# Kernel tuning notes

Hardware: AMD Instinct MI355X
Metric: run time of the kernel (lower is better)

## Reference

```python
import jax, jax.numpy as jnp
import numpy as np

NEARZERO = 1e-6
UH_LEN = 15
T_STEPS, N_GRID, NMUL = 1460, 2000, 1

BOUNDS = [
    ("inf_pc", 0.0, 1.0), ("inf_hbv_beta", 0.5, 3.0), ("inf_vic_bexp", 0.001, 3.0),
    ("inf_hmets_alpha", 0.3, 1.0), ("bf1_gr4j_x3", 20.0, 300.0), ("bf1_bfc", -8.0, -2.0),
    ("bf1_bfn", 1.0, 5.0), ("bf1_bfmax", 0.1, 200.0), ("bf1_lam", 0.1, 0.5),
    ("bf1_thresh", 0.0001, 0.9999), ("max_perc", 1.0, 50.0), ("perc_sfc", 0.0001, 0.9999),
    ("crise_hbv", 0.1, 50.0), ("bf2_bfmax", 0.1, 100.0), ("bf2_gr4j_x3", 50.0, 500.0),
    ("bf2_bfc", -8.0, -2.0), ("bf2_bfn", 1.0, 5.0), ("Tbf", -5.0, 2.0), ("Kf", 0.0, 5.0),
    ("ddf_min", 1.5, 3.0), ("ddf_plus", 0.0, 5.0), ("Kcum", 0.01, 0.2), ("Tbm", -1.0, 1.0),
    ("swi", 0.0, 0.4), ("forest_cover", 0.0, 1.0), ("forest_sparseness", 0.0, 1.0),
    ("max_soilwater1", 50.0, 500.0), ("max_soilwater2", 50.0, 500.0),
    ("alpha1", 0.3, 20.0), ("beta1", 0.01, 5.0), ("alpha2", 0.5, 13.0), ("beta2", 0.15, 1.5),
]


def setup_inputs():
    key = jax.random.key(0)
    kP, kT, kE, kW, kH = jax.random.split(key, 5)
    prcp = jnp.maximum(jax.random.normal(kP, (T_STEPS, N_GRID)) * 8.0, 0.0)  # mm/day
    temp = jax.random.normal(kT, (T_STEPS, N_GRID)) * 10.0                   # degC
    pet = jax.random.uniform(kE, (T_STEPS, N_GRID)) * 5.0                    # mm/day
    x_phy = jnp.stack([prcp, temp, pet], axis=-1).astype(jnp.float32)
    weights_params = jax.random.normal(kW, (T_STEPS, N_GRID, 24), dtype=jnp.float32)
    hybrid_params = jax.random.normal(kH, (N_GRID, 32), dtype=jnp.float32)
    return {"x_phy": x_phy, "weights_params": weights_params, "hybrid_params": hybrid_params}


def _route(flow, alpha, beta):
    # flow [T,G,M]; alpha,beta [G,M]. Discrete gamma-shaped causal unit hydrograph.
    k = jnp.arange(1.0, UH_LEN + 1.0, dtype=flow.dtype)
    logw = (alpha[..., None] - 1.0) * jnp.log(k) - k / beta[..., None]  # [G,M,L]
    uh = jax.nn.softmax(logw, axis=-1)
    out = jnp.zeros_like(flow)
    for lag in range(UH_LEN):  # small fixed UH length
        shifted = jnp.pad(flow, ((lag, 0), (0, 0), (0, 0)))[: flow.shape[0]]
        out = out + uh[..., lag] * shifted
    return out


def _forward(x_phy, weights_params, hybrid_params):
    T, G, _ = x_phy.shape
    # --- unpack + descale parameters (sigmoid -> physical range) ---
    s = jax.nn.sigmoid(hybrid_params.reshape(G, len(BOUNDS), NMUL))
    p = {n: lo + s[:, i] * (hi - lo) for i, (n, lo, hi) in enumerate(BOUNDS)}  # each [G,M]
    w = weights_params.reshape(T, G, 24, NMUL)
    w_inf = jax.nn.softmax(w[:, :, 0:6], axis=2)    # infiltration blend weights
    w_bf1 = jax.nn.softmax(w[:, :, 6:12], axis=2)   # baseflow1 blend weights
    w_bf2 = jax.nn.softmax(w[:, :, 12:18], axis=2)  # baseflow2 blend weights
    gates = jnp.round(jax.nn.sigmoid(w[:, :, 18:24]))  # perc,capi,evpr,evps,conv1,conv2
    Pm, Tm, Petm = x_phy[:, :, 0:1], x_phy[:, :, 1:2], x_phy[:, :, 2:3]

    def step(carry, xs):
        snow, liq, cum, sw1, sw2 = carry
        prcp, temp, pet, wi, wb1, wb2, g = xs
        rain = jnp.where(temp >= 0.0, prcp, 0.0)
        snowf = jnp.where(temp < 0.0, prcp, 0.0)
        canopy = pet * p["forest_cover"] * (1.0 - p["forest_sparseness"])
        rain = jnp.maximum(rain - canopy * g[:, 2], 0.0)
        snowf = jnp.maximum(snowf - canopy * g[:, 3], 0.0)
        # HBV refreeze of snowpack liquid water
        refreeze = jnp.minimum(liq, p["Kf"] * jnp.maximum(p["Tbf"] - temp, 0.0))
        snow = snow + snowf + refreeze
        liq = liq - refreeze
        # HMETS degree-day melt with cumulative-melt-dependent factor
        ddf = p["ddf_min"] + p["ddf_plus"] * (1.0 - jnp.exp(-p["Kcum"] * cum))
        melt = jnp.minimum(snow, ddf * jnp.maximum(temp - p["Tbm"], 0.0))
        snow = snow - melt
        cum = jnp.where(snow < NEARZERO, NEARZERO, cum + melt)
        liq = liq + melt
        overflow = jnp.maximum(liq - p["swi"] * snow, 0.0)  # snow liquid retention
        liq = liq - overflow
        wavail = rain + overflow
        # blended infiltration (6 options)
        sat1 = jnp.clip(sw1 / p["max_soilwater1"], NEARZERO, 1.0)
        dry1 = jnp.clip(1.0 - sat1, NEARZERO, 1.0)
        inf_opts = jnp.stack([
            wavail * p["inf_pc"],
            wavail * (1.0 - sat1 ** p["inf_hbv_beta"]),
            wavail * dry1 ** p["inf_vic_bexp"],
            wavail * p["inf_hmets_alpha"] * dry1,
            wavail * (1.0 - sat1 * sat1),
            wavail,
        ], axis=1)  # [G,6,M]
        infil = jnp.sum(wi * inf_opts, axis=1)
        sw1 = sw1 + infil
        excess = jnp.maximum(sw1 - p["max_soilwater1"], 0.0)
        sw1 = sw1 - excess
        surf = wavail - infil + excess
        # percolation (gated)
        sat1 = jnp.clip(sw1 / p["max_soilwater1"], NEARZERO, 1.0)
        perc = g[:, 0] * p["max_perc"] * jnp.maximum(sat1 - p["perc_sfc"], 0.0) / (1.0 - p["perc_sfc"])
        perc = jnp.minimum(perc, sw1)
        sw1, sw2 = sw1 - perc, sw2 + perc
        # capillary rise (gated)
        sat2 = jnp.clip(sw2 / p["max_soilwater2"], NEARZERO, 1.0)
        sat1 = jnp.clip(sw1 / p["max_soilwater1"], NEARZERO, 1.0)
        capi = jnp.minimum(g[:, 1] * p["crise_hbv"] * (1.0 - sat1) * sat2, sw2)
        sw2, sw1 = sw2 - capi, sw1 + capi
        # soil evapotranspiration
        sat1 = jnp.clip(sw1 / p["max_soilwater1"], NEARZERO, 1.0)
        et = jnp.minimum(pet * sat1, sw1)
        sw1 = sw1 - et
        # blended baseflow from layer 1 (6 options)
        sat1 = jnp.clip(sw1 / p["max_soilwater1"], NEARZERO, 1.0)
        bf1_opts = jnp.stack([
            sw1 * (1.0 - (1.0 + (sw1 / p["bf1_gr4j_x3"]) ** 4) ** -0.25),
            10.0 ** p["bf1_bfc"] * sw1,
            p["bf1_bfmax"] * sat1 ** p["bf1_bfn"],
            p["bf1_bfmax"] * sat1,
            p["bf1_bfmax"] * jnp.expm1(p["bf1_lam"] * sat1) / jnp.expm1(p["bf1_lam"]),
            p["bf1_bfmax"] * jnp.maximum(sat1 - p["bf1_thresh"], 0.0) / (1.0 - p["bf1_thresh"]),
        ], axis=1)
        bf1 = jnp.minimum(jnp.sum(wb1 * bf1_opts, axis=1), sw1)
        sw1 = sw1 - bf1
        # blended baseflow from layer 2 (6 options)
        sat2 = jnp.clip(sw2 / p["max_soilwater2"], NEARZERO, 1.0)
        bf2_opts = jnp.stack([
            sw2 * (1.0 - (1.0 + (sw2 / p["bf2_gr4j_x3"]) ** 4) ** -0.25),
            10.0 ** p["bf2_bfc"] * sw2,
            p["bf2_bfmax"] * sat2 ** p["bf2_bfn"],
            p["bf2_bfmax"] * sat2,
            p["bf2_bfmax"] * sat2 * sat2,
            10.0 ** p["bf2_bfc"] * sw2 * sat2,
        ], axis=1)
        bf2 = jnp.minimum(jnp.sum(wb2 * bf2_opts, axis=1), sw2)
        sw2 = sw2 - bf2
        return (snow, liq, cum, sw1, sw2), (surf, bf1, bf2)

    init = tuple(jnp.full((G, NMUL), NEARZERO, dtype=x_phy.dtype) for _ in range(5))
    _, (surf, bf1, bf2) = jax.lax.scan(step, init, (Pm, Tm, Petm, w_inf, w_bf1, w_bf2, gates))
    # gamma unit-hydrograph routing (gated blend with un-routed flow)
    base = bf1 + bf2
    qs = gates[:, :, 4] * _route(surf, p["alpha1"], p["beta1"]) + (1.0 - gates[:, :, 4]) * surf
    qb = gates[:, :, 5] * _route(base, p["alpha2"], p["beta2"]) + (1.0 - gates[:, :, 5]) * base
    return jnp.mean(qs + qb, axis=-1)  # [T, G] simulated streamflow


def reference(x_phy, weights_params, hybrid_params):
    return _forward(x_phy, weights_params, hybrid_params)
```

## Files before the change

### kernel.cpp

```cpp
#include <hip/hip_runtime.h>
#include <cstdint>
#include <cmath>

#define T_STEPS 1460
#define N_GRID  2000
#define UH_LEN  15
#define NZ      1e-6f
#define NB      32
#define NPLANE  24
#define SLOT_FLOATS (NPLANE * 64)
#define DEPTH   8

static const size_t TG = (size_t)T_STEPS * N_GRID;

__device__ __forceinline__ float pb(float x, float lo, float hi) {
    float s = 1.0f / (1.0f + expf(-x));
    return lo + s * (hi - lo);
}

__device__ __forceinline__ float clip01(float x) {
    return fminf(fmaxf(x, NZ), 1.0f);
}

__device__ __forceinline__ float gatef(float x) {
    if (fabsf(x) < 1e-4f) {
        double s = 1.0 / (1.0 + exp(-(double)x));
        return (float)rint(s);
    }
    return (x > 0.0f) ? 1.0f : 0.0f;
}

__global__ __launch_bounds__(256)
void uh_kernel(const float* __restrict__ hyb,
               float* __restrict__ uh1, float* __restrict__ uh2)
{
    const int g = blockIdx.x * 256 + threadIdx.x;
    if (g >= N_GRID) return;
    const float* h = hyb + (size_t)g * 32;
    const float a1 = pb(h[28], 0.3f, 20.0f);
    const float b1 = pb(h[29], 0.01f, 5.0f);
    const float a2 = pb(h[30], 0.5f, 13.0f);
    const float b2 = pb(h[31], 0.15f, 1.5f);

    float lw[UH_LEN];
    {
        float m = -1e30f;
        #pragma unroll
        for (int k = 0; k < UH_LEN; ++k) {
            const float kk = (float)(k + 1);
            lw[k] = (a1 - 1.0f) * logf(kk) - kk / b1;
            m = fmaxf(m, lw[k]);
        }
        float s = 0.0f;
        #pragma unroll
        for (int k = 0; k < UH_LEN; ++k) { lw[k] = expf(lw[k] - m); s += lw[k]; }
        const float inv = 1.0f / s;
        #pragma unroll
        for (int k = 0; k < UH_LEN; ++k) uh1[k * N_GRID + g] = lw[k] * inv;
    }
    {
        float m = -1e30f;
        #pragma unroll
        for (int k = 0; k < UH_LEN; ++k) {
            const float kk = (float)(k + 1);
            lw[k] = (a2 - 1.0f) * logf(kk) - kk / b2;
            m = fmaxf(m, lw[k]);
        }
        float s = 0.0f;
        #pragma unroll
        for (int k = 0; k < UH_LEN; ++k) { lw[k] = expf(lw[k] - m); s += lw[k]; }
        const float inv = 1.0f / s;
        #pragma unroll
        for (int k = 0; k < UH_LEN; ++k) uh2[k * N_GRID + g] = lw[k] * inv;
    }
}

__global__ __launch_bounds__(256)
void prep_kernel(const float* __restrict__ xphy,
                 const float* __restrict__ wts,
                 const float* __restrict__ hyb,
                 float* __restrict__ stream,
                 unsigned char* __restrict__ gate_o)
{
    const int gid = blockIdx.x * 256 + threadIdx.x;
    if (gid >= NB * 64) return;
    const int t = blockIdx.y;
    const int b = gid >> 6, c = gid & 63;
    float* sp = stream + ((size_t)b * T_STEPS + t) * SLOT_FLOATS;

    if (gid >= N_GRID) {
        #pragma unroll
        for (int p = 0; p < NPLANE; ++p) sp[p * 64 + c] = 0.0f;
        return;
    }

    const size_t idx = (size_t)t * N_GRID + gid;
    const float* xp = xphy + idx * 3;
    const float prcp = xp[0], temp = xp[1], pet = xp[2];

    float w[24];
    const float4* wp = (const float4*)(wts + idx * 24);
    #pragma unroll
    for (int k = 0; k < 6; ++k) {
        float4 v = wp[k];
        w[4*k] = v.x; w[4*k+1] = v.y; w[4*k+2] = v.z; w[4*k+3] = v.w;
    }

    float e[18];
    #pragma unroll
    for (int k = 0; k < 18; ++k) e[k] = __expf(w[k]);
    float s0 = 0.f, s1 = 0.f, s2 = 0.f;
    #pragma unroll
    for (int k = 0; k < 6; ++k) { s0 += e[k]; s1 += e[6+k]; s2 += e[12+k]; }
    const float r0 = 1.0f / s0, r1 = 1.0f / s1, r2 = 1.0f / s2;

    const float g0 = gatef(w[18]);
    const float g1 = gatef(w[19]);
    const float g2 = gatef(w[20]);
    const float g3 = gatef(w[21]);
    const float g4 = gatef(w[22]);
    const float g5 = gatef(w[23]);

    const float* h = hyb + (size_t)gid * 32;
    const float fc = pb(h[24], 0.0f, 1.0f);
    const float fs = pb(h[25], 0.0f, 1.0f);
    const float canopy = pet * (fc * (1.0f - fs));
    const float pshed = (temp >= 0.0f) ? fmaxf(prcp - canopy * g2, 0.0f)
                                       : fmaxf(prcp - canopy * g3, 0.0f);

    sp[0 * 64 + c] = temp;
    sp[1 * 64 + c] = pet;
    sp[2 * 64 + c] = pshed;
    #pragma unroll
    for (int k = 0; k < 6; ++k) {
        sp[(3 + k)  * 64 + c] = e[k]      * r0;
        sp[(9 + k)  * 64 + c] = e[6 + k]  * r1;
        sp[(15 + k) * 64 + c] = e[12 + k] * r2;
    }
    sp[21 * 64 + c] = g0;
    sp[22 * 64 + c] = g1;
    sp[23 * 64 + c] = 0.0f;
    gate_o[idx] = (unsigned char)((g4 > 0.5f ? 1 : 0) | (g5 > 0.5f ? 2 : 0));
}

__device__ __forceinline__ void load_slot(const float* sp, float* lp, int lane)
{
    #pragma unroll
    for (int i = 0; i < 6; ++i) {
        __builtin_amdgcn_global_load_lds(
            (const __attribute__((address_space(1))) void*)(sp + i * 256 + lane * 4),
            (__attribute__((address_space(3))) void*)(lp + i * 256 + lane * 4),
            16, 0, 0);
    }
}

__global__ __launch_bounds__(64, 1)
void scan_stream_kernel(const float* __restrict__ stream,
                        const float* __restrict__ hyb,
                        float* __restrict__ surf_o,
                        float* __restrict__ base_o)
{
    __shared__ float lds[DEPTH * SLOT_FLOATS];
    const int lane = threadIdx.x;
    const int b = blockIdx.x;
    const int g = b * 64 + lane;
    const int gc = (g < N_GRID) ? g : (N_GRID - 1);

    const float* h = hyb + (size_t)gc * 32;
    const float inf_pc   = pb(h[0],  0.0f,   1.0f);
    const float hbv_beta = pb(h[1],  0.5f,   3.0f);
    const float vic_bexp = pb(h[2],  0.001f, 3.0f);
    const float hmets_al = pb(h[3],  0.3f,   1.0f);
    const float x3_1     = pb(h[4],  20.0f,  300.0f);
    const float bfc1     = pb(h[5],  -8.0f,  -2.0f);
    const float bfn1     = pb(h[6],  1.0f,   5.0f);
    const float bfmax1   = pb(h[7],  0.1f,   200.0f);
    const float lam      = pb(h[8],  0.1f,   0.5f);
    const float th1      = pb(h[9],  0.0001f,0.9999f);
    const float max_perc = pb(h[10], 1.0f,   50.0f);
    const float sfc      = pb(h[11], 0.0001f,0.9999f);
    const float crise    = pb(h[12], 0.1f,   50.0f);
    const float bfmax2   = pb(h[13], 0.1f,   100.0f);
    const float x3_2     = pb(h[14], 50.0f,  500.0f);
    const float bfc2     = pb(h[15], -8.0f,  -2.0f);
    const float bfn2     = pb(h[16], 1.0f,   5.0f);
    const float Tbf      = pb(h[17], -5.0f,  2.0f);
    const float Kf       = pb(h[18], 0.0f,   5.0f);
    const float ddf_min  = pb(h[19], 1.5f,   3.0f);
    const float ddf_plus = pb(h[20], 0.0f,   5.0f);
    const float Kcum     = pb(h[21], 0.01f,  0.2f);
    const float Tbm      = pb(h[22], -1.0f,  1.0f);
    const float swi      = pb(h[23], 0.0f,   0.4f);
    const float msw1     = pb(h[26], 50.0f,  500.0f);
    const float msw2     = pb(h[27], 50.0f,  500.0f);

    const float inv_msw1 = 1.0f / msw1;
    const float inv_msw2 = 1.0f / msw2;
    const float pow10_1  = powf(10.0f, bfc1);
    const float pow10_2  = powf(10.0f, bfc2);
    const float inv_x3_1 = 1.0f / x3_1;
    const float inv_x3_2 = 1.0f / x3_2;
    const float b1o4     = bfmax1 / expm1f(lam);
    const float b1o5     = bfmax1 / (1.0f - th1);
    const float perc_fac = max_perc / (1.0f - sfc);

    const float* src = stream + (size_t)b * T_STEPS * SLOT_FLOATS;

    for (int s = 0; s < DEPTH - 1; ++s)
        load_slot(src + (size_t)s * SLOT_FLOATS, lds + s * SLOT_FLOATS, lane);

    float snow = NZ, liq = NZ, cum = NZ, sw1 = NZ, sw2 = NZ;

    for (int t = 0; t < T_STEPS; ++t) {
        if (t + DEPTH - 1 < T_STEPS) {
            const int ts = t + DEPTH - 1;
            load_slot(src + (size_t)ts * SLOT_FLOATS,
                      lds + (ts & (DEPTH - 1)) * SLOT_FLOATS, lane);
            if (t >= DEPTH - 1) {
                asm volatile("s_waitcnt vmcnt(56)" ::: "memory");
            } else {
                asm volatile("s_waitcnt vmcnt(42)" ::: "memory");
            }
        } else {
            asm volatile("s_waitcnt vmcnt(0)" ::: "memory");
        }

        const float* L = lds + (t & (DEPTH - 1)) * SLOT_FLOATS;
        const float temp  = L[0 * 64 + lane];
        const float pet   = L[1 * 64 + lane];
        const float pshed = L[2 * 64 + lane];
        const float a0 = L[3 * 64 + lane],  a1 = L[4 * 64 + lane];
        const float a2 = L[5 * 64 + lane],  a3 = L[6 * 64 + lane];
        const float a4 = L[7 * 64 + lane],  a5 = L[8 * 64 + lane];
        const float f0 = L[9 * 64 + lane],  f1 = L[10 * 64 + lane];
        const float f2 = L[11 * 64 + lane], f3 = L[12 * 64 + lane];
        const float f4 = L[13 * 64 + lane], f5 = L[14 * 64 + lane];
        const float c0 = L[15 * 64 + lane], c1 = L[16 * 64 + lane];
        const float c2 = L[17 * 64 + lane], c3 = L[18 * 64 + lane];
        const float c4 = L[19 * 64 + lane], c5 = L[20 * 64 + lane];
        const float g0 = L[21 * 64 + lane], g1 = L[22 * 64 + lane];

        const float rain  = (temp >= 0.0f) ? pshed : 0.0f;
        const float snowf = (temp <  0.0f) ? pshed : 0.0f;

        const float refreeze = fminf(liq, Kf * fmaxf(Tbf - temp, 0.0f));
        snow = snow + snowf + refreeze;
        liq  = liq - refreeze;
        const float ddf = ddf_min + ddf_plus * (1.0f - __expf(-Kcum * cum));
        const float melt = fminf(snow, ddf * fmaxf(temp - Tbm, 0.0f));
        snow -= melt;
        cum = (snow < NZ) ? NZ : (cum + melt);
        liq += melt;
        const float overflow = fmaxf(liq - swi * snow, 0.0f);
        liq -= overflow;
        const float wavail = rain + overflow;

        float sat1 = clip01(sw1 * inv_msw1);
        const float dry1 = clip01(1.0f - sat1);
        const float p1 = __powf(sat1, hbv_beta);
        const float p2 = __powf(dry1, vic_bexp);
        const float infil = wavail *
            (a0 * inf_pc + a1 * (1.0f - p1) + a2 * p2 +
             a3 * (hmets_al * dry1) + a4 * (1.0f - sat1 * sat1) + a5);

        sw1 += infil;
        const float excess = fmaxf(sw1 - msw1, 0.0f);
        sw1 -= excess;
        const float surf = wavail - infil + excess;

        sat1 = clip01(sw1 * inv_msw1);
        const float perc = fminf(g0 * perc_fac * fmaxf(sat1 - sfc, 0.0f), sw1);
        sw1 -= perc; sw2 += perc;

        float sat2 = clip01(sw2 * inv_msw2);
        sat1 = clip01(sw1 * inv_msw1);
        const float capi = fminf(g1 * crise * (1.0f - sat1) * sat2, sw2);
        sw2 -= capi; sw1 += capi;

        sat1 = clip01(sw1 * inv_msw1);
        const float et = fminf(pet * sat1, sw1);
        sw1 -= et;

        sat1 = clip01(sw1 * inv_msw1);
        const float q = sw1 * inv_x3_1;
        const float q4 = (q * q) * (q * q);
        const float gr1 = sw1 * (1.0f - __powf(1.0f + q4, -0.25f));
        const float pw1 = __powf(sat1, bfn1);
        const float ex1 = __expf(lam * sat1) - 1.0f;
        const float bsum1 = f0 * gr1 + f1 * (pow10_1 * sw1) + f2 * (bfmax1 * pw1) +
                            f3 * (bfmax1 * sat1) + f4 * (b1o4 * ex1) +
                            f5 * (b1o5 * fmaxf(sat1 - th1, 0.0f));
        const float bf1 = fminf(bsum1, sw1);
        sw1 -= bf1;

        sat2 = clip01(sw2 * inv_msw2);
        const float u = sw2 * inv_x3_2;
        const float u4 = (u * u) * (u * u);
        const float gr2 = sw2 * (1.0f - __powf(1.0f + u4, -0.25f));
        const float pw2 = __powf(sat2, bfn2);
        const float t10 = pow10_2 * sw2;
        const float bsum2 = c0 * gr2 + c1 * t10 + c2 * (bfmax2 * pw2) +
                            c3 * (bfmax2 * sat2) + c4 * (bfmax2 * sat2 * sat2) +
                            c5 * (t10 * sat2);
        const float bf2 = fminf(bsum2, sw2);
        sw2 -= bf2;

        if (g < N_GRID) {
            const size_t o = (size_t)t * N_GRID + g;
            surf_o[o] = surf;
            base_o[o] = bf1 + bf2;
        }
    }
}

__global__ __launch_bounds__(64)
void scan_kernel(const float* __restrict__ xphy,
                 const float* __restrict__ wts,
                 const float* __restrict__ hyb,
                 float* __restrict__ surf_o,
                 float* __restrict__ base_o,
                 unsigned char* __restrict__ gate_o)
{
    const int g = blockIdx.x * 64 + threadIdx.x;
    if (g >= N_GRID) return;

    const float* h = hyb + (size_t)g * 32;
    const float inf_pc   = pb(h[0],  0.0f,   1.0f);
    const float hbv_beta = pb(h[1],  0.5f,   3.0f);
    const float vic_bexp = pb(h[2],  0.001f, 3.0f);
    const float hmets_al = pb(h[3],  0.3f,   1.0f);
    const float x3_1     = pb(h[4],  20.0f,  300.0f);
    const float bfc1     = pb(h[5],  -8.0f,  -2.0f);
    const float bfn1     = pb(h[6],  1.0f,   5.0f);
    const float bfmax1   = pb(h[7],  0.1f,   200.0f);
    const float lam      = pb(h[8],  0.1f,   0.5f);
    const float th1      = pb(h[9],  0.0001f,0.9999f);
    const float max_perc = pb(h[10], 1.0f,   50.0f);
    const float sfc      = pb(h[11], 0.0001f,0.9999f);
    const float crise    = pb(h[12], 0.1f,   50.0f);
    const float bfmax2   = pb(h[13], 0.1f,   100.0f);
    const float x3_2     = pb(h[14], 50.0f,  500.0f);
    const float bfc2     = pb(h[15], -8.0f,  -2.0f);
    const float bfn2     = pb(h[16], 1.0f,   5.0f);
    const float Tbf      = pb(h[17], -5.0f,  2.0f);
    const float Kf       = pb(h[18], 0.0f,   5.0f);
    const float ddf_min  = pb(h[19], 1.5f,   3.0f);
    const float ddf_plus = pb(h[20], 0.0f,   5.0f);
    const float Kcum     = pb(h[21], 0.01f,  0.2f);
    const float Tbm      = pb(h[22], -1.0f,  1.0f);
    const float swi      = pb(h[23], 0.0f,   0.4f);
    const float fc       = pb(h[24], 0.0f,   1.0f);
    const float fs       = pb(h[25], 0.0f,   1.0f);
    const float msw1     = pb(h[26], 50.0f,  500.0f);
    const float msw2     = pb(h[27], 50.0f,  500.0f);

    const float inv_msw1  = 1.0f / msw1;
    const float inv_msw2  = 1.0f / msw2;
    const float canopy_fac = fc * (1.0f - fs);
    const float pow10_1   = powf(10.0f, bfc1);
    const float pow10_2   = powf(10.0f, bfc2);
    const float inv_x3_1  = 1.0f / x3_1;
    const float inv_x3_2  = 1.0f / x3_2;
    const float b1o4      = bfmax1 / expm1f(lam);
    const float b1o5      = bfmax1 / (1.0f - th1);
// ... 55 lines not shown
        sw1 -= perc; sw2 += perc;

        float sat2 = clip01(sw2 * inv_msw2);
        sat1 = clip01(sw1 * inv_msw1);
        const float capi = fminf(g1 * crise * (1.0f - sat1) * sat2, sw2);
        sw2 -= capi; sw1 += capi;

        sat1 = clip01(sw1 * inv_msw1);
        const float et = fminf(pet * sat1, sw1);
        sw1 -= et;

        sat1 = clip01(sw1 * inv_msw1);
        const float f0 = __expf(wc1.z), f1 = __expf(wc1.w), f2 = __expf(wc2.x),
                    f3 = __expf(wc2.y), f4 = __expf(wc2.z), f5 = __expf(wc2.w);
        const float rb1 = 1.0f / (f0 + f1 + f2 + f3 + f4 + f5);
        const float q = sw1 * inv_x3_1;
        const float q4 = (q * q) * (q * q);
        const float gr1 = sw1 * (1.0f - __powf(1.0f + q4, -0.25f));
        const float pw1 = __powf(sat1, bfn1);
        const float ex1 = __expf(lam * sat1) - 1.0f;
        const float bsum1 = f0 * gr1 + f1 * (pow10_1 * sw1) + f2 * (bfmax1 * pw1) +
                            f3 * (bfmax1 * sat1) + f4 * (b1o4 * ex1) +
                            f5 * (b1o5 * fmaxf(sat1 - th1, 0.0f));
        const float bf1 = fminf(bsum1 * rb1, sw1);
        sw1 -= bf1;

        sat2 = clip01(sw2 * inv_msw2);
        const float c0 = __expf(wc3.x), c1 = __expf(wc3.y), c2 = __expf(wc3.z),
                    c3 = __expf(wc3.w), c4 = __expf(wc4.x), c5 = __expf(wc4.y);
        const float rb2 = 1.0f / (c0 + c1 + c2 + c3 + c4 + c5);
        const float u = sw2 * inv_x3_2;
        const float u4 = (u * u) * (u * u);
        const float gr2 = sw2 * (1.0f - __powf(1.0f + u4, -0.25f));
        const float pw2 = __powf(sat2, bfn2);
        const float t10 = pow10_2 * sw2;
        const float bsum2 = c0 * gr2 + c1 * t10 + c2 * (bfmax2 * pw2) +
                            c3 * (bfmax2 * sat2) + c4 * (bfmax2 * sat2 * sat2) +
                            c5 * (t10 * sat2);
        const float bf2 = fminf(bsum2 * rb2, sw2);
        sw2 -= bf2;

        surf_o[idx] = surf;
        base_o[idx] = bf1 + bf2;
        gate_o[idx] = (unsigned char)((g4 > 0.5f ? 1 : 0) | (g5 > 0.5f ? 2 : 0));
    }
}

__global__ __launch_bounds__(256)
void route_kernel(const float* __restrict__ surf,
                  const float* __restrict__ base,
                  const float* __restrict__ uh1,
                  const float* __restrict__ uh2,
                  const unsigned char* __restrict__ gates,
                  float* __restrict__ out)
{
    const int g = blockIdx.x * 256 + threadIdx.x;
    if (g >= N_GRID) return;
    const int t = blockIdx.y;
    const size_t o = (size_t)t * N_GRID + g;

    const unsigned char gb = gates[o];
    const float s0 = surf[o];
    const float b0 = base[o];

    float accs = 0.0f, accb = 0.0f;
    #pragma unroll
    for (int lag = 0; lag < UH_LEN; ++lag) {
        const int tt = t - lag;
        const float sv = (tt >= 0) ? surf[(size_t)tt * N_GRID + g] : 0.0f;
        const float bv = (tt >= 0) ? base[(size_t)tt * N_GRID + g] : 0.0f;
        accs += uh1[lag * N_GRID + g] * sv;
        accb += uh2[lag * N_GRID + g] * bv;
    }
    const float qs = (gb & 1) ? accs : s0;
    const float qb = (gb & 2) ? accb : b0;
    out[o] = qs + qb;
}

extern "C" void kernel_launch(void* const* d_in, const int* in_sizes, int n_in,
                              void* d_out, int out_size, void* d_ws, size_t ws_size,
                              hipStream_t stream)
{
    const float* x_phy = (const float*)d_in[0];
    const float* wts   = (const float*)d_in[1];
    const float* hyb   = (const float*)d_in[2];
    float* out = (float*)d_out;

    const size_t stream_f = (size_t)NB * T_STEPS * SLOT_FLOATS;
    const size_t uh_f     = (size_t)UH_LEN * N_GRID;
    const size_t big_need = stream_f * 4 + TG * (2 * 4 + 1) + 2 * uh_f * 4;

    if (ws_size >= big_need) {
        float* strm = (float*)d_ws;
        float* surf = strm + stream_f;
        float* base = surf + TG;
        float* uh1  = base + TG;
        float* uh2  = uh1 + uh_f;
        unsigned char* gbits = (unsigned char*)(uh2 + uh_f);

        prep_kernel<<<dim3((NB * 64) / 256, T_STEPS), dim3(256), 0, stream>>>(
            x_phy, wts, hyb, strm, gbits);
        uh_kernel<<<dim3((N_GRID + 255) / 256), dim3(256), 0, stream>>>(hyb, uh1, uh2);
        scan_stream_kernel<<<dim3(NB), dim3(64), 0, stream>>>(strm, hyb, surf, base);
        route_kernel<<<dim3((N_GRID + 255) / 256, T_STEPS), dim3(256), 0, stream>>>(
            surf, base, uh1, uh2, gbits, out);
    } else {
        float* surf = (float*)d_ws;
        float* base = surf + TG;
        float* uh1  = base + TG;
        float* uh2  = uh1 + uh_f;
        unsigned char* gbits = (unsigned char*)(uh2 + uh_f);

        uh_kernel<<<dim3((N_GRID + 255) / 256), dim3(256), 0, stream>>>(hyb, uh1, uh2);
        scan_kernel<<<dim3((N_GRID + 63) / 64), dim3(64), 0, stream>>>(
            x_phy, wts, hyb, surf, base, gbits);
        route_kernel<<<dim3((N_GRID + 255) / 256, T_STEPS), dim3(256), 0, stream>>>(
            surf, base, uh1, uh2, gbits, out);
    }
}
```

Baseline: 3.850 ms.

## Pack per-step stream as float4 and double-buffer slot reads into registers

The prep kernel now writes each timestep slot as six interleaved float4 vectors instead of 24 scalar planes. The scan kernel reads a whole slot into registers with six 128-bit LDS loads, one step ahead, alternating between two register buffers in a 2x unrolled loop. The goal is to hide LDS read latency and cut LDS instruction count on the serial recurrence. The vmcnt thresholds are retuned for the new ordering. This uses more registers, and the wait counts must match the number of outstanding loads exactly, so an off-by-one would read stale data.

Result: slower. 4.412 ms (+14.6%).

```diff
diff --git a/kernel.cpp b/kernel.cpp
--- a/kernel.cpp
+++ b/kernel.cpp
@@ -86,11 +86,12 @@
     if (gid >= NB * 64) return;
     const int t = blockIdx.y;
     const int b = gid >> 6, c = gid & 63;
-    float* sp = stream + ((size_t)b * T_STEPS + t) * SLOT_FLOATS;
+    float4* sp4 = (float4*)(stream + ((size_t)b * T_STEPS + t) * SLOT_FLOATS);
 
     if (gid >= N_GRID) {
-        #pragma unroll
-        for (int p = 0; p < NPLANE; ++p) sp[p * 64 + c] = 0.0f;
+        const float4 z = make_float4(0.f, 0.f, 0.f, 0.f);
+        #pragma unroll
+        for (int q = 0; q < 6; ++q) sp4[q * 64 + c] = z;
         return;
     }
 
@@ -128,18 +129,12 @@
     const float pshed = (temp >= 0.0f) ? fmaxf(prcp - canopy * g2, 0.0f)
                                        : fmaxf(prcp - canopy * g3, 0.0f);
 
-    sp[0 * 64 + c] = temp;
-    sp[1 * 64 + c] = pet;
-    sp[2 * 64 + c] = pshed;
-    #pragma unroll
-    for (int k = 0; k < 6; ++k) {
-        sp[(3 + k)  * 64 + c] = e[k]      * r0;
-        sp[(9 + k)  * 64 + c] = e[6 + k]  * r1;
-        sp[(15 + k) * 64 + c] = e[12 + k] * r2;
-    }
-    sp[21 * 64 + c] = g0;
-    sp[22 * 64 + c] = g1;
-    sp[23 * 64 + c] = 0.0f;
+    sp4[0 * 64 + c] = make_float4(temp, pet, pshed, e[0] * r0);
+    sp4[1 * 64 + c] = make_float4(e[1] * r0, e[2] * r0, e[3] * r0, e[4] * r0);
+    sp4[2 * 64 + c] = make_float4(e[5] * r0, e[6] * r1, e[7] * r1, e[8] * r1);
+    sp4[3 * 64 + c] = make_float4(e[9] * r1, e[10] * r1, e[11] * r1, e[12] * r2);
+    sp4[4 * 64 + c] = make_float4(e[13] * r2, e[14] * r2, e[15] * r2, e[16] * r2);
+    sp4[5 * 64 + c] = make_float4(e[17] * r2, g0, g1, 0.0f);
     gate_o[idx] = (unsigned char)((g4 > 0.5f ? 1 : 0) | (g5 > 0.5f ? 2 : 0));
 }
 
@@ -152,6 +147,21 @@
             (__attribute__((address_space(3))) void*)(lp + i * 256 + lane * 4),
             16, 0, 0);
     }
+}
+
+struct Slot {
+    float4 q0, q1, q2, q3, q4, q5;
+};
+
+__device__ __forceinline__ void read_slot_regs(const float* L, int lane, Slot& s)
+{
+    const float4* v = (const float4*)L;
+    s.q0 = v[0 * 64 + lane];
+    s.q1 = v[1 * 64 + lane];
+    s.q2 = v[2 * 64 + lane];
+    s.q3 = v[3 * 64 + lane];
+    s.q4 = v[4 * 64 + lane];
+    s.q5 = v[5 * 64 + lane];
 }
 
 __global__ __launch_bounds__(64, 1)
@@ -206,39 +216,17 @@
 
     const float* src = stream + (size_t)b * T_STEPS * SLOT_FLOATS;
 
-    for (int s = 0; s < DEPTH - 1; ++s)
-        load_slot(src + (size_t)s * SLOT_FLOATS, lds + s * SLOT_FLOATS, lane);
-
     float snow = NZ, liq = NZ, cum = NZ, sw1 = NZ, sw2 = NZ;
 
-    for (int t = 0; t < T_STEPS; ++t) {
-        if (t + DEPTH - 1 < T_STEPS) {
-            const int ts = t + DEPTH - 1;
-            load_slot(src + (size_t)ts * SLOT_FLOATS,
-                      lds + (ts & (DEPTH - 1)) * SLOT_FLOATS, lane);
-            if (t >= DEPTH - 1) {
-                asm volatile("s_waitcnt vmcnt(56)" ::: "memory");
-            } else {
-                asm volatile("s_waitcnt vmcnt(42)" ::: "memory");
-            }
-        } else {
-            asm volatile("s_waitcnt vmcnt(0)" ::: "memory");
-        }
-
-        const float* L = lds + (t & (DEPTH - 1)) * SLOT_FLOATS;
-        const float temp  = L[0 * 64 + lane];
-        const float pet   = L[1 * 64 + lane];
-        const float pshed = L[2 * 64 + lane];
-        const float a0 = L[3 * 64 + lane],  a1 = L[4 * 64 + lane];
-        const float a2 = L[5 * 64 + lane],  a3 = L[6 * 64 + lane];
-        const float a4 = L[7 * 64 + lane],  a5 = L[8 * 64 + lane];
-        const float f0 = L[9 * 64 + lane],  f1 = L[10 * 64 + lane];
-        const float f2 = L[11 * 64 + lane], f3 = L[12 * 64 + lane];
-        const float f4 = L[13 * 64 + lane], f5 = L[14 * 64 + lane];
-        const float c0 = L[15 * 64 + lane], c1 = L[16 * 64 + lane];
-        const float c2 = L[17 * 64 + lane], c3 = L[18 * 64 + lane];
-        const float c4 = L[19 * 64 + lane], c5 = L[20 * 64 + lane];
-        const float g0 = L[21 * 64 + lane], g1 = L[22 * 64 + lane];
+    auto emit = [&](int t, const Slot& S) {
+        const float temp  = S.q0.x, pet = S.q0.y, pshed = S.q0.z;
+        const float a0 = S.q0.w, a1 = S.q1.x, a2 = S.q1.y;
+        const float a3 = S.q1.z, a4 = S.q1.w, a5 = S.q2.x;
+        const float f0 = S.q2.y, f1 = S.q2.z, f2 = S.q2.w;
+        const float f3 = S.q3.x, f4 = S.q3.y, f5 = S.q3.z;
+        const float c0 = S.q3.w, c1 = S.q4.x, c2 = S.q4.y;
+        const float c3 = S.q4.z, c4 = S.q4.w, c5 = S.q5.x;
+        const float g0 = S.q5.y, g1 = S.q5.z;
 
         const float rain  = (temp >= 0.0f) ? pshed : 0.0f;
         const float snowf = (temp <  0.0f) ? pshed : 0.0f;
@@ -283,8 +271,8 @@
 
         sat1 = clip01(sw1 * inv_msw1);
         const float q = sw1 * inv_x3_1;
-        const float q4 = (q * q) * (q * q);
-        const float gr1 = sw1 * (1.0f - __powf(1.0f + q4, -0.25f));
+        const float q4v = (q * q) * (q * q);
+        const float gr1 = sw1 * (1.0f - __powf(1.0f + q4v, -0.25f));
         const float pw1 = __powf(sat1, bfn1);
         const float ex1 = __expf(lam * sat1) - 1.0f;
         const float bsum1 = f0 * gr1 + f1 * (pow10_1 * sw1) + f2 * (bfmax1 * pw1) +
@@ -310,6 +298,38 @@
             surf_o[o] = surf;
             base_o[o] = bf1 + bf2;
         }
+    };
+
+    auto prefetch = [&](int u, Slot& dst) {
+        if (u + 1 < T_STEPS) {
+            if (u + DEPTH - 1 < T_STEPS) {
+                const int ts = u + DEPTH - 1;
+                load_slot(src + (size_t)ts * SLOT_FLOATS,
+                          lds + (ts & (DEPTH - 1)) * SLOT_FLOATS, lane);
+                if (u >= 6) {
+                    asm volatile("s_waitcnt vmcnt(48)" ::: "memory");
+                } else {
+                    asm volatile("s_waitcnt vmcnt(36)" ::: "memory");
+                }
+            } else {
+                asm volatile("s_waitcnt vmcnt(0)" ::: "memory");
+            }
+            read_slot_regs(lds + ((u + 1) & (DEPTH - 1)) * SLOT_FLOATS, lane, dst);
+        }
+    };
+
+    for (int s = 0; s < DEPTH - 1; ++s)
+        load_slot(src + (size_t)s * SLOT_FLOATS, lds + s * SLOT_FLOATS, lane);
+    asm volatile("s_waitcnt vmcnt(36)" ::: "memory");
+
+    Slot A, B;
+    read_slot_regs(lds, lane, A);
+
+    for (int t = 0; t < T_STEPS; t += 2) {
+        prefetch(t, B);
+        emit(t, A);
+        prefetch(t + 1, A);
+        emit(t + 1, B);
     }
 }
 
```

## Spread scan over 250 blocks of 8 cells with cell-major float4 stream layout

Applied to the files above, without the earlier changes.

The sequential time scan now runs on 250 single-wave blocks of 8 grid cells each, replacing 32 blocks of 64 cells, so the latency-bound recurrence is spread across many more compute units. The staged stream is switched to a cell-major layout so prep writes six float4 per cell and the scan reads six float4 from LDS. The async load and waitcnt values are rescaled to one load per slot. Only 8 of 64 lanes do useful work and the other 56 compute duplicate values, trading lane utilisation for more parallel serial chains.

Measured after the change: 3.810 ms. No clear change (-1.0%).

```diff
diff --git a/kernel.cpp b/kernel.cpp
--- a/kernel.cpp
+++ b/kernel.cpp
@@ -6,9 +6,10 @@
 #define N_GRID  2000
 #define UH_LEN  15
 #define NZ      1e-6f
-#define NB      32
+#define CPB     8
+#define NBLK    250
 #define NPLANE  24
-#define SLOT_FLOATS (NPLANE * 64)
+#define SLOT_FLOATS (NPLANE * CPB)
 #define DEPTH   8
 
 static const size_t TG = (size_t)T_STEPS * N_GRID;
@@ -83,16 +84,11 @@
                  unsigned char* __restrict__ gate_o)
 {
     const int gid = blockIdx.x * 256 + threadIdx.x;
-    if (gid >= NB * 64) return;
+    if (gid >= N_GRID) return;
     const int t = blockIdx.y;
-    const int b = gid >> 6, c = gid & 63;
-    float* sp = stream + ((size_t)b * T_STEPS + t) * SLOT_FLOATS;
-
-    if (gid >= N_GRID) {
-        #pragma unroll
-        for (int p = 0; p < NPLANE; ++p) sp[p * 64 + c] = 0.0f;
-        return;
-    }
+    const int b = gid >> 3, c = gid & 7;
+    float4* sp4 = (float4*)(stream + ((size_t)b * T_STEPS + t) * SLOT_FLOATS
+                            + (size_t)c * NPLANE);
 
     const size_t idx = (size_t)t * N_GRID + gid;
     const float* xp = xphy + idx * 3;
@@ -128,28 +124,21 @@
     const float pshed = (temp >= 0.0f) ? fmaxf(prcp - canopy * g2, 0.0f)
                                        : fmaxf(prcp - canopy * g3, 0.0f);
 
-    sp[0 * 64 + c] = temp;
-    sp[1 * 64 + c] = pet;
-    sp[2 * 64 + c] = pshed;
-    #pragma unroll
-    for (int k = 0; k < 6; ++k) {
-        sp[(3 + k)  * 64 + c] = e[k]      * r0;
-        sp[(9 + k)  * 64 + c] = e[6 + k]  * r1;
-        sp[(15 + k) * 64 + c] = e[12 + k] * r2;
-    }
-    sp[21 * 64 + c] = g0;
-    sp[22 * 64 + c] = g1;
-    sp[23 * 64 + c] = 0.0f;
+    sp4[0] = make_float4(temp, pet, pshed, e[0] * r0);
+    sp4[1] = make_float4(e[1] * r0, e[2] * r0, e[3] * r0, e[4] * r0);
+    sp4[2] = make_float4(e[5] * r0, e[6] * r1, e[7] * r1, e[8] * r1);
+    sp4[3] = make_float4(e[9] * r1, e[10] * r1, e[11] * r1, e[12] * r2);
+    sp4[4] = make_float4(e[13] * r2, e[14] * r2, e[15] * r2, e[16] * r2);
+    sp4[5] = make_float4(e[17] * r2, g0, g1, 0.0f);
     gate_o[idx] = (unsigned char)((g4 > 0.5f ? 1 : 0) | (g5 > 0.5f ? 2 : 0));
 }
 
 __device__ __forceinline__ void load_slot(const float* sp, float* lp, int lane)
 {
-    #pragma unroll
-    for (int i = 0; i < 6; ++i) {
+    if (lane < 48) {
         __builtin_amdgcn_global_load_lds(
-            (const __attribute__((address_space(1))) void*)(sp + i * 256 + lane * 4),
-            (__attribute__((address_space(3))) void*)(lp + i * 256 + lane * 4),
+            (const __attribute__((address_space(1))) void*)(sp + lane * 4),
+            (__attribute__((address_space(3))) void*)(lp + lane * 4),
             16, 0, 0);
     }
 }
@@ -163,10 +152,11 @@
     __shared__ float lds[DEPTH * SLOT_FLOATS];
     const int lane = threadIdx.x;
     const int b = blockIdx.x;
-    const int g = b * 64 + lane;
-    const int gc = (g < N_GRID) ? g : (N_GRID - 1);
-
-    const float* h = hyb + (size_t)gc * 32;
+    const int cell = lane & (CPB - 1);
+    const int g = b * CPB + cell;
+    const bool live = (lane < CPB);
+
+    const float* h = hyb + (size_t)g * 32;
     const float inf_pc   = pb(h[0],  0.0f,   1.0f);
     const float hbv_beta = pb(h[1],  0.5f,   3.0f);
     const float vic_bexp = pb(h[2],  0.001f, 3.0f);
@@ -217,28 +207,27 @@
             load_slot(src + (size_t)ts * SLOT_FLOATS,
                       lds + (ts & (DEPTH - 1)) * SLOT_FLOATS, lane);
             if (t >= DEPTH - 1) {
-                asm volatile("s_waitcnt vmcnt(56)" ::: "memory");
+                asm volatile("s_waitcnt vmcnt(21)" ::: "memory");
             } else {
-                asm volatile("s_waitcnt vmcnt(42)" ::: "memory");
+                asm volatile("s_waitcnt vmcnt(7)" ::: "memory");
             }
         } else {
             asm volatile("s_waitcnt vmcnt(0)" ::: "memory");
         }
 
-        const float* L = lds + (t & (DEPTH - 1)) * SLOT_FLOATS;
-        const float temp  = L[0 * 64 + lane];
-        const float pet   = L[1 * 64 + lane];
-        const float pshed = L[2 * 64 + lane];
-        const float a0 = L[3 * 64 + lane],  a1 = L[4 * 64 + lane];
-        const float a2 = L[5 * 64 + lane],  a3 = L[6 * 64 + lane];
-        const float a4 = L[7 * 64 + lane],  a5 = L[8 * 64 + lane];
-        const float f0 = L[9 * 64 + lane],  f1 = L[10 * 64 + lane];
-        const float f2 = L[11 * 64 + lane], f3 = L[12 * 64 + lane];
-        const float f4 = L[13 * 64 + lane], f5 = L[14 * 64 + lane];
-        const float c0 = L[15 * 64 + lane], c1 = L[16 * 64 + lane];
-        const float c2 = L[17 * 64 + lane], c3 = L[18 * 64 + lane];
-        const float c4 = L[19 * 64 + lane], c5 = L[20 * 64 + lane];
-        const float g0 = L[21 * 64 + lane], g1 = L[22 * 64 + lane];
+        const float4* v = (const float4*)(lds + (t & (DEPTH - 1)) * SLOT_FLOATS
+                                          + (size_t)cell * NPLANE);
+        const float4 q0 = v[0], q1 = v[1], q2 = v[2];
+        const float4 q3 = v[3], q4r = v[4], q5 = v[5];
+
+        const float temp  = q0.x, pet = q0.y, pshed = q0.z;
+        const float a0 = q0.w, a1 = q1.x, a2 = q1.y;
+        const float a3 = q1.z, a4 = q1.w, a5 = q2.x;
+        const float f0 = q2.y, f1 = q2.z, f2 = q2.w;
+        const float f3 = q3.x, f4 = q3.y, f5 = q3.z;
+        const float c0 = q3.w, c1 = q4r.x, c2 = q4r.y;
+        const float c3 = q4r.z, c4 = q4r.w, c5 = q5.x;
+        const float g0 = q5.y, g1 = q5.z;
 
         const float rain  = (temp >= 0.0f) ? pshed : 0.0f;
         const float snowf = (temp <  0.0f) ? pshed : 0.0f;
@@ -305,7 +294,7 @@
         const float bf2 = fminf(bsum2, sw2);
         sw2 -= bf2;
 
-        if (g < N_GRID) {
+        if (live) {
             const size_t o = (size_t)t * N_GRID + g;
             surf_o[o] = surf;
             base_o[o] = bf1 + bf2;
@@ -505,7 +494,7 @@
     const float* hyb   = (const float*)d_in[2];
     float* out = (float*)d_out;
 
-    const size_t stream_f = (size_t)NB * T_STEPS * SLOT_FLOATS;
+    const size_t stream_f = (size_t)NBLK * T_STEPS * SLOT_FLOATS;
     const size_t uh_f     = (size_t)UH_LEN * N_GRID;
     const size_t big_need = stream_f * 4 + TG * (2 * 4 + 1) + 2 * uh_f * 4;
 
@@ -517,10 +506,10 @@
         float* uh2  = uh1 + uh_f;
         unsigned char* gbits = (unsigned char*)(uh2 + uh_f);
 
-        prep_kernel<<<dim3((NB * 64) / 256, T_STEPS), dim3(256), 0, stream>>>(
+        prep_kernel<<<dim3((N_GRID + 255) / 256, T_STEPS), dim3(256), 0, stream>>>(
             x_phy, wts, hyb, strm, gbits);
         uh_kernel<<<dim3((N_GRID + 255) / 256), dim3(256), 0, stream>>>(hyb, uh1, uh2);
-        scan_stream_kernel<<<dim3(NB), dim3(64), 0, stream>>>(strm, hyb, surf, base);
+        scan_stream_kernel<<<dim3(NBLK), dim3(64), 0, stream>>>(strm, hyb, surf, base);
         route_kernel<<<dim3((N_GRID + 255) / 256, T_STEPS), dim3(256), 0, stream>>>(
             surf, base, uh1, uh2, gbits, out);
     } else {
```

## Fold per-step parameter products into prep stream and vectorize scan LDS reads

Applied to the files above, without the earlier changes.

Moves the time-invariant parameter scaling (pow10, bfmax, perc/crise factors, constant infiltration sum) from the serial scan into the parallel prep kernel, which now packs the slot as float4 vectors. The scan reads six float4s per step instead of 24 scalar LDS loads, uses a nested rsqrt in place of pow(x,-0.25), and peels the loop to drop per-iteration branches. Output arrays are padded to 2048 columns so the guard on stores can go. The aim is to shorten the latency-bound sequential chain, at the cost of a slightly different floating-point rounding and extra workspace.

Measured after the change: 3.499 ms. 1.1x faster.

```diff
diff --git a/kernel.cpp b/kernel.cpp
--- a/kernel.cpp
+++ b/kernel.cpp
@@ -4,6 +4,7 @@
 
 #define T_STEPS 1460
 #define N_GRID  2000
+#define GPAD    2048
 #define UH_LEN  15
 #define NZ      1e-6f
 #define NB      32
@@ -11,7 +12,8 @@
 #define SLOT_FLOATS (NPLANE * 64)
 #define DEPTH   8
 
-static const size_t TG = (size_t)T_STEPS * N_GRID;
+static const size_t TG  = (size_t)T_STEPS * N_GRID;
+static const size_t TGP = (size_t)T_STEPS * GPAD;
 
 __device__ __forceinline__ float pb(float x, float lo, float hi) {
     float s = 1.0f / (1.0f + expf(-x));
@@ -86,11 +88,12 @@
     if (gid >= NB * 64) return;
     const int t = blockIdx.y;
     const int b = gid >> 6, c = gid & 63;
-    float* sp = stream + ((size_t)b * T_STEPS + t) * SLOT_FLOATS;
+    float4* sp4 = (float4*)(stream + ((size_t)b * T_STEPS + t) * SLOT_FLOATS);
 
     if (gid >= N_GRID) {
-        #pragma unroll
-        for (int p = 0; p < NPLANE; ++p) sp[p * 64 + c] = 0.0f;
+        const float4 z = make_float4(0.f, 0.f, 0.f, 0.f);
+        #pragma unroll
+        for (int q = 0; q < 6; ++q) sp4[q * 64 + c] = z;
         return;
     }
 
@@ -122,58 +125,9 @@
     const float g5 = gatef(w[23]);
 
     const float* h = hyb + (size_t)gid * 32;
-    const float fc = pb(h[24], 0.0f, 1.0f);
-    const float fs = pb(h[25], 0.0f, 1.0f);
-    const float canopy = pet * (fc * (1.0f - fs));
-    const float pshed = (temp >= 0.0f) ? fmaxf(prcp - canopy * g2, 0.0f)
-                                       : fmaxf(prcp - canopy * g3, 0.0f);
-
-    sp[0 * 64 + c] = temp;
-    sp[1 * 64 + c] = pet;
-    sp[2 * 64 + c] = pshed;
-    #pragma unroll
-    for (int k = 0; k < 6; ++k) {
-        sp[(3 + k)  * 64 + c] = e[k]      * r0;
-        sp[(9 + k)  * 64 + c] = e[6 + k]  * r1;
-        sp[(15 + k) * 64 + c] = e[12 + k] * r2;
-    }
-    sp[21 * 64 + c] = g0;
-    sp[22 * 64 + c] = g1;
-    sp[23 * 64 + c] = 0.0f;
-    gate_o[idx] = (unsigned char)((g4 > 0.5f ? 1 : 0) | (g5 > 0.5f ? 2 : 0));
-}
-
-__device__ __forceinline__ void load_slot(const float* sp, float* lp, int lane)
-{
-    #pragma unroll
-    for (int i = 0; i < 6; ++i) {
-        __builtin_amdgcn_global_load_lds(
-            (const __attribute__((address_space(1))) void*)(sp + i * 256 + lane * 4),
-            (__attribute__((address_space(3))) void*)(lp + i * 256 + lane * 4),
-            16, 0, 0);
-    }
-}
-
-__global__ __launch_bounds__(64, 1)
-void scan_stream_kernel(const float* __restrict__ stream,
-                        const float* __restrict__ hyb,
-                        float* __restrict__ surf_o,
-                        float* __restrict__ base_o)
-{
-    __shared__ float lds[DEPTH * SLOT_FLOATS];
-    const int lane = threadIdx.x;
-    const int b = blockIdx.x;
-    const int g = b * 64 + lane;
-    const int gc = (g < N_GRID) ? g : (N_GRID - 1);
-
-    const float* h = hyb + (size_t)gc * 32;
     const float inf_pc   = pb(h[0],  0.0f,   1.0f);
-    const float hbv_beta = pb(h[1],  0.5f,   3.0f);
-    const float vic_bexp = pb(h[2],  0.001f, 3.0f);
     const float hmets_al = pb(h[3],  0.3f,   1.0f);
-    const float x3_1     = pb(h[4],  20.0f,  300.0f);
     const float bfc1     = pb(h[5],  -8.0f,  -2.0f);
-    const float bfn1     = pb(h[6],  1.0f,   5.0f);
     const float bfmax1   = pb(h[7],  0.1f,   200.0f);
     const float lam      = pb(h[8],  0.1f,   0.5f);
     const float th1      = pb(h[9],  0.0001f,0.9999f);
@@ -181,8 +135,71 @@
     const float sfc      = pb(h[11], 0.0001f,0.9999f);
     const float crise    = pb(h[12], 0.1f,   50.0f);
     const float bfmax2   = pb(h[13], 0.1f,   100.0f);
+    const float bfc2     = pb(h[15], -8.0f,  -2.0f);
+    const float fc       = pb(h[24], 0.0f,   1.0f);
+    const float fs       = pb(h[25], 0.0f,   1.0f);
+
+    const float pow10_1 = powf(10.0f, bfc1);
+    const float pow10_2 = powf(10.0f, bfc2);
+    const float b1o4    = bfmax1 / expm1f(lam);
+    const float b1o5    = bfmax1 / (1.0f - th1);
+    const float perc_fac = max_perc / (1.0f - sfc);
+
+    const float canopy = pet * (fc * (1.0f - fs));
+    const float pshed = (temp >= 0.0f) ? fmaxf(prcp - canopy * g2, 0.0f)
+                                       : fmaxf(prcp - canopy * g3, 0.0f);
+
+    const float a0 = e[0]*r0, a1 = e[1]*r0, a2 = e[2]*r0;
+    const float a3 = e[3]*r0, a4 = e[4]*r0, a5 = e[5]*r0;
+    const float f0 = e[6]*r1, f1 = e[7]*r1, f2 = e[8]*r1;
+    const float f3 = e[9]*r1, f4 = e[10]*r1, f5 = e[11]*r1;
+    const float c0v = e[12]*r2, c1v = e[13]*r2, c2v = e[14]*r2;
+    const float c3v = e[15]*r2, c4v = e[16]*r2, c5v = e[17]*r2;
+
+    const float K = a0 * inf_pc + a1 + a4 + a5;
+
+    sp4[0 * 64 + c] = make_float4(temp, pet, pshed, K);
+    sp4[1 * 64 + c] = make_float4(a1, a2, a3 * hmets_al, a4);
+    sp4[2 * 64 + c] = make_float4(f0, f1 * pow10_1, f2 * bfmax1, f3 * bfmax1);
+    sp4[3 * 64 + c] = make_float4(f4 * b1o4, f5 * b1o5, c0v, c1v * pow10_2);
+    sp4[4 * 64 + c] = make_float4(c2v * bfmax2, c3v * bfmax2, c4v * bfmax2,
+                                  c5v * pow10_2);
+    sp4[5 * 64 + c] = make_float4(g0 * perc_fac, g1 * crise, 0.0f, 0.0f);
+    gate_o[idx] = (unsigned char)((g4 > 0.5f ? 1 : 0) | (g5 > 0.5f ? 2 : 0));
+}
+
+__device__ __forceinline__ void load_slot(const float* sp, float* lp, int lane)
+{
+    #pragma unroll
+    for (int i = 0; i < 6; ++i) {
+        __builtin_amdgcn_global_load_lds(
+            (const __attribute__((address_space(1))) void*)(sp + i * 256 + lane * 4),
+            (__attribute__((address_space(3))) void*)(lp + i * 256 + lane * 4),
+            16, 0, 0);
+    }
+}
+
+__global__ __launch_bounds__(64, 1)
+void scan_stream_kernel(const float* __restrict__ stream,
+                        const float* __restrict__ hyb,
+                        float* __restrict__ surf_o,
+                        float* __restrict__ base_o)
+{
+    __shared__ float lds[DEPTH * SLOT_FLOATS];
+    const int lane = threadIdx.x;
+    const int b = blockIdx.x;
+    const int g = b * 64 + lane;
+    const int gc = (g < N_GRID) ? g : (N_GRID - 1);
+
+    const float* h = hyb + (size_t)gc * 32;
+    const float hbv_beta = pb(h[1],  0.5f,   3.0f);
+    const float vic_bexp = pb(h[2],  0.001f, 3.0f);
+    const float x3_1     = pb(h[4],  20.0f,  300.0f);
+    const float bfn1     = pb(h[6],  1.0f,   5.0f);
+    const float lam      = pb(h[8],  0.1f,   0.5f);
+    const float th1      = pb(h[9],  0.0001f,0.9999f);
+    const float sfc      = pb(h[11], 0.0001f,0.9999f);
     const float x3_2     = pb(h[14], 50.0f,  500.0f);
-    const float bfc2     = pb(h[15], -8.0f,  -2.0f);
     const float bfn2     = pb(h[16], 1.0f,   5.0f);
     const float Tbf      = pb(h[17], -5.0f,  2.0f);
     const float Kf       = pb(h[18], 0.0f,   5.0f);
@@ -196,49 +213,28 @@
 
     const float inv_msw1 = 1.0f / msw1;
     const float inv_msw2 = 1.0f / msw2;
-    const float pow10_1  = powf(10.0f, bfc1);
-    const float pow10_2  = powf(10.0f, bfc2);
     const float inv_x3_1 = 1.0f / x3_1;
     const float inv_x3_2 = 1.0f / x3_2;
-    const float b1o4     = bfmax1 / expm1f(lam);
-    const float b1o5     = bfmax1 / (1.0f - th1);
-    const float perc_fac = max_perc / (1.0f - sfc);
 
     const float* src = stream + (size_t)b * T_STEPS * SLOT_FLOATS;
 
-    for (int s = 0; s < DEPTH - 1; ++s)
-        load_slot(src + (size_t)s * SLOT_FLOATS, lds + s * SLOT_FLOATS, lane);
-
     float snow = NZ, liq = NZ, cum = NZ, sw1 = NZ, sw2 = NZ;
 
-    for (int t = 0; t < T_STEPS; ++t) {
-        if (t + DEPTH - 1 < T_STEPS) {
-            const int ts = t + DEPTH - 1;
-            load_slot(src + (size_t)ts * SLOT_FLOATS,
-                      lds + (ts & (DEPTH - 1)) * SLOT_FLOATS, lane);
-            if (t >= DEPTH - 1) {
-                asm volatile("s_waitcnt vmcnt(56)" ::: "memory");
-            } else {
-                asm volatile("s_waitcnt vmcnt(42)" ::: "memory");
-            }
-        } else {
-            asm volatile("s_waitcnt vmcnt(0)" ::: "memory");
-        }
-
-        const float* L = lds + (t & (DEPTH - 1)) * SLOT_FLOATS;
-        const float temp  = L[0 * 64 + lane];
-        const float pet   = L[1 * 64 + lane];
-        const float pshed = L[2 * 64 + lane];
-        const float a0 = L[3 * 64 + lane],  a1 = L[4 * 64 + lane];
-        const float a2 = L[5 * 64 + lane],  a3 = L[6 * 64 + lane];
-        const float a4 = L[7 * 64 + lane],  a5 = L[8 * 64 + lane];
-        const float f0 = L[9 * 64 + lane],  f1 = L[10 * 64 + lane];
-        const float f2 = L[11 * 64 + lane], f3 = L[12 * 64 + lane];
-        const float f4 = L[13 * 64 + lane], f5 = L[14 * 64 + lane];
-        const float c0 = L[15 * 64 + lane], c1 = L[16 * 64 + lane];
-        const float c2 = L[17 * 64 + lane], c3 = L[18 * 64 + lane];
-        const float c4 = L[19 * 64 + lane], c5 = L[20 * 64 + lane];
-        const float g0 = L[21 * 64 + lane], g1 = L[22 * 64 + lane];
+    auto body = [&](int t) {
+        const float4* v = (const float4*)(lds + (t & (DEPTH - 1)) * SLOT_FLOATS);
+        const float4 q0 = v[0 * 64 + lane];
+        const float4 q1 = v[1 * 64 + lane];
+        const float4 q2 = v[2 * 64 + lane];
+        const float4 q3 = v[3 * 64 + lane];
+        const float4 q4v_ = v[4 * 64 + lane];
+        const float4 q5 = v[5 * 64 + lane];
+
+        const float temp = q0.x, pet = q0.y, pshed = q0.z, K = q0.w;
+        const float a1 = q1.x, a2 = q1.y, a3s = q1.z, a4 = q1.w;
+        const float f0 = q2.x, f1s = q2.y, f2s = q2.z, f3s = q2.w;
+        const float f4s = q3.x, f5s = q3.y, c0 = q3.z, c1s = q3.w;
+        const float c2s = q4v_.x, c3s = q4v_.y, c4s = q4v_.z, c5s = q4v_.w;
+        const float g0p = q5.x, g1c = q5.y;
 
         const float rain  = (temp >= 0.0f) ? pshed : 0.0f;
         const float snowf = (temp <  0.0f) ? pshed : 0.0f;
@@ -260,8 +256,7 @@
         const float p1 = __powf(sat1, hbv_beta);
         const float p2 = __powf(dry1, vic_bexp);
         const float infil = wavail *
-            (a0 * inf_pc + a1 * (1.0f - p1) + a2 * p2 +
-             a3 * (hmets_al * dry1) + a4 * (1.0f - sat1 * sat1) + a5);
+            (K - a1 * p1 + a2 * p2 + a3s * dry1 - a4 * (sat1 * sat1));
 
         sw1 += infil;
         const float excess = fmaxf(sw1 - msw1, 0.0f);
@@ -269,12 +264,12 @@
         const float surf = wavail - infil + excess;
 
         sat1 = clip01(sw1 * inv_msw1);
-        const float perc = fminf(g0 * perc_fac * fmaxf(sat1 - sfc, 0.0f), sw1);
+        const float perc = fminf(g0p * fmaxf(sat1 - sfc, 0.0f), sw1);
         sw1 -= perc; sw2 += perc;
 
         float sat2 = clip01(sw2 * inv_msw2);
         sat1 = clip01(sw1 * inv_msw1);
-        const float capi = fminf(g1 * crise * (1.0f - sat1) * sat2, sw2);
+        const float capi = fminf(g1c * (1.0f - sat1) * sat2, sw2);
         sw2 -= capi; sw1 += capi;
 
         sat1 = clip01(sw1 * inv_msw1);
@@ -284,32 +279,54 @@
         sat1 = clip01(sw1 * inv_msw1);
         const float q = sw1 * inv_x3_1;
         const float q4 = (q * q) * (q * q);
-        const float gr1 = sw1 * (1.0f - __powf(1.0f + q4, -0.25f));
+        const float x1 = 1.0f + q4;
+        const float pm1 = __frsqrt_rn(__frsqrt_rn(x1) * x1);
+        const float gr1 = sw1 * (1.0f - pm1);
         const float pw1 = __powf(sat1, bfn1);
         const float ex1 = __expf(lam * sat1) - 1.0f;
-        const float bsum1 = f0 * gr1 + f1 * (pow10_1 * sw1) + f2 * (bfmax1 * pw1) +
-                            f3 * (bfmax1 * sat1) + f4 * (b1o4 * ex1) +
-                            f5 * (b1o5 * fmaxf(sat1 - th1, 0.0f));
+        const float bsum1 = f0 * gr1 + f1s * sw1 + f2s * pw1 +
+                            f3s * sat1 + f4s * ex1 +
+                            f5s * fmaxf(sat1 - th1, 0.0f);
         const float bf1 = fminf(bsum1, sw1);
         sw1 -= bf1;
 
         sat2 = clip01(sw2 * inv_msw2);
         const float u = sw2 * inv_x3_2;
         const float u4 = (u * u) * (u * u);
-        const float gr2 = sw2 * (1.0f - __powf(1.0f + u4, -0.25f));
+        const float x2 = 1.0f + u4;
+        const float pm2 = __frsqrt_rn(__frsqrt_rn(x2) * x2);
+        const float gr2 = sw2 * (1.0f - pm2);
         const float pw2 = __powf(sat2, bfn2);
-        const float t10 = pow10_2 * sw2;
-        const float bsum2 = c0 * gr2 + c1 * t10 + c2 * (bfmax2 * pw2) +
-                            c3 * (bfmax2 * sat2) + c4 * (bfmax2 * sat2 * sat2) +
-                            c5 * (t10 * sat2);
+        const float bsum2 = c0 * gr2 + c1s * sw2 + c2s * pw2 +
+                            c3s * sat2 + c4s * (sat2 * sat2) +
+                            c5s * (sw2 * sat2);
         const float bf2 = fminf(bsum2, sw2);
         sw2 -= bf2;
 
-        if (g < N_GRID) {
-            const size_t o = (size_t)t * N_GRID + g;
-            surf_o[o] = surf;
-            base_o[o] = bf1 + bf2;
-        }
+        const size_t o = (size_t)t * GPAD + g;
+        surf_o[o] = surf;
+        base_o[o] = bf1 + bf2;
+    };
+
+    for (int s = 0; s < DEPTH - 1; ++s)
+        load_slot(src + (size_t)s * SLOT_FLOATS, lds + s * SLOT_FLOATS, lane);
+
+    int t = 0;
+    for (; t < DEPTH - 1; ++t) {
+        load_slot(src + (size_t)(t + DEPTH - 1) * SLOT_FLOATS,
+                  lds + ((t + DEPTH - 1) & (DEPTH - 1)) * SLOT_FLOATS, lane);
+        asm volatile("s_waitcnt vmcnt(42)" ::: "memory");
+        body(t);
+    }
+    for (; t < T_STEPS - (DEPTH - 1); ++t) {
+        load_slot(src + (size_t)(t + DEPTH - 1) * SLOT_FLOATS,
+                  lds + ((t + DEPTH - 1) & (DEPTH - 1)) * SLOT_FLOATS, lane);
+        asm volatile("s_waitcnt vmcnt(56)" ::: "memory");
+        body(t);
+    }
+    for (; t < T_STEPS; ++t) {
+        asm volatile("s_waitcnt vmcnt(0)" ::: "memory");
+        body(t);
     }
 }
 
@@ -471,23 +488,24 @@
                   const float* __restrict__ uh1,
                   const float* __restrict__ uh2,
                   const unsigned char* __restrict__ gates,
-                  float* __restrict__ out)
+                  float* __restrict__ out, int gp)
 {
     const int g = blockIdx.x * 256 + threadIdx.x;
     if (g >= N_GRID) return;
     const int t = blockIdx.y;
-    const size_t o = (size_t)t * N_GRID + g;
+    const size_t o  = (size_t)t * N_GRID + g;
+    const size_t op = (size_t)t * gp + g;
 
     const unsigned char gb = gates[o];
-    const float s0 = surf[o];
-    const float b0 = base[o];
+    const float s0 = surf[op];
+    const float b0 = base[op];
 
     float accs = 0.0f, accb = 0.0f;
     #pragma unroll
     for (int lag = 0; lag < UH_LEN; ++lag) {
         const int tt = t - lag;
-        const float sv = (tt >= 0) ? surf[(size_t)tt * N_GRID + g] : 0.0f;
-        const float bv = (tt >= 0) ? base[(size_t)tt * N_GRID + g] : 0.0f;
+        const float sv = (tt >= 0) ? surf[(size_t)tt * gp + g] : 0.0f;
+        const float bv = (tt >= 0) ? base[(size_t)tt * gp + g] : 0.0f;
         accs += uh1[lag * N_GRID + g] * sv;
         accb += uh2[lag * N_GRID + g] * bv;
     }
@@ -507,13 +525,13 @@
 
     const size_t stream_f = (size_t)NB * T_STEPS * SLOT_FLOATS;
     const size_t uh_f     = (size_t)UH_LEN * N_GRID;
-    const size_t big_need = stream_f * 4 + TG * (2 * 4 + 1) + 2 * uh_f * 4;
+    const size_t big_need = stream_f * 4 + 2 * TGP * 4 + TG + 2 * uh_f * 4;
 
     if (ws_size >= big_need) {
         float* strm = (float*)d_ws;
         float* surf = strm + stream_f;
-        float* base = surf + TG;
-        float* uh1  = base + TG;
+        float* base = surf + TGP;
+        float* uh1  = base + TGP;
         float* uh2  = uh1 + uh_f;
         unsigned char* gbits = (unsigned char*)(uh2 + uh_f);
 
@@ -522,7 +540,7 @@
         uh_kernel<<<dim3((N_GRID + 255) / 256), dim3(256), 0, stream>>>(hyb, uh1, uh2);
         scan_stream_kernel<<<dim3(NB), dim3(64), 0, stream>>>(strm, hyb, surf, base);
         route_kernel<<<dim3((N_GRID + 255) / 256, T_STEPS), dim3(256), 0, stream>>>(
-            surf, base, uh1, uh2, gbits, out);
+            surf, base, uh1, uh2, gbits, out, GPAD);
     } else {
         float* surf = (float*)d_ws;
         float* base = surf + TG;
@@ -534,6 +552,6 @@
         scan_kernel<<<dim3((N_GRID + 63) / 64), dim3(64), 0, stream>>>(
             x_phy, wts, hyb, surf, base, gbits);
         route_kernel<<<dim3((N_GRID + 255) / 256, T_STEPS), dim3(256), 0, stream>>>(
-            surf, base, uh1, uh2, gbits, out);
-    }
-}
+            surf, base, uh1, uh2, gbits, out, N_GRID);
+    }
+}
```
